# Performance work log

Measured on AMD Instinct MI355X. Metric: run time of the kernel, lower is better.

The kernel has to match this reference:

```python
import jax, jax.numpy as jnp
import numpy as np

NUM_HEADS = 16


def setup_inputs() -> dict:
    key = jax.random.key(0)
    k1, k2, k3, k4 = jax.random.split(key, 4)
    B, N, C = 2, 2048, 1024
    x = jax.random.normal(k1, (B, N, C), dtype=jnp.float32)
    mask = jax.random.randint(k2, (B, N), 0, 2) > 0  # bool [B, N]
    # torch Linear weights: y = x @ W.T
    w_qkv = jax.random.normal(k3, (3 * C, C), dtype=jnp.float32) * (C ** -0.5)
    w_proj = jax.random.normal(k4, (C, C), dtype=jnp.float32) * (C ** -0.5)
    b_proj = jnp.zeros((C,), dtype=jnp.float32)
    return {"x": x, "mask": mask, "w_qkv": w_qkv, "w_proj": w_proj, "b_proj": b_proj}


def reference(x, mask, w_qkv, w_proj, b_proj):
    B, N, C = x.shape
    H = NUM_HEADS
    D = C // H
    scale = D ** -0.5
    qkv = x @ w_qkv.T                                   # [B, N, 3C]
    qkv = qkv.reshape(B, N, 3, H, D).transpose(2, 0, 3, 1, 4)  # [3, B, H, N, D]
    q, k, v = qkv[0], qkv[1], qkv[2]
    attn = jnp.einsum('bhnd,bhmd->bhnm', q, k) * scale  # [B, H, N, N]
    mask_value = -jnp.finfo(attn.dtype).max
    m2 = mask[:, None, :] & mask[:, :, None]            # [B, N, N]
    attn = jnp.where(m2[:, None, :, :], attn, mask_value)
    attn = jax.nn.softmax(attn, axis=-1)
    # dropout layers are identity in eval mode
    out = jnp.einsum('bhnm,bhmd->bhnd', attn, v)        # [B, H, N, D]
    out = out.transpose(0, 2, 1, 3).reshape(B, N, C)
    out = out @ w_proj.T + b_proj
    return out
```

## Files before the change

kernel.cpp:

```cpp
#include <hip/hip_runtime.h>

typedef unsigned short u16;
typedef unsigned int   u32;
typedef short  short8 __attribute__((ext_vector_type(8)));
typedef float  f32x4  __attribute__((ext_vector_type(4)));
typedef float  f32x16 __attribute__((ext_vector_type(16)));
typedef u16    u16x4  __attribute__((ext_vector_type(4)));

__device__ __forceinline__ u16 f2b(float f) {
    u32 u = __float_as_uint(f);
    u32 r = (u + 0x7fffu + ((u >> 16) & 1u)) >> 16;
    return (u16)r;
}

__device__ __forceinline__ u32 cvtpk(float a, float b) {
    u32 r;
    asm("v_cvt_pk_bf16_f32 %0, %1, %2" : "=v"(r) : "v"(a), "v"(b));
    return r;
}

__device__ __forceinline__ void gload_lds16(const void* g, void* l) {
    __builtin_amdgcn_global_load_lds(
        (const __attribute__((address_space(1))) u32*)g,
        (__attribute__((address_space(3))) u32*)l,
        16, 0, 0);
}

__global__ void cvt_bf16(const float* __restrict__ src, u16* __restrict__ dst, int n4) {
    int i = blockIdx.x * blockDim.x + threadIdx.x;
    if (i >= n4) return;
    float4 v = ((const float4*)src)[i];
    u16x4 r = { f2b(v.x), f2b(v.y), f2b(v.z), f2b(v.w) };
    ((u16x4*)dst)[i] = r;
}

__global__ __launch_bounds__(256) void gemm_bt(
    const u16* __restrict__ A, const u16* __restrict__ Bm,
    u16* __restrict__ Cb, float* __restrict__ Cf, const float* __restrict__ bias,
    int M, int N, int K)
{
    __shared__ __align__(16) u16 As[128*32];
    __shared__ __align__(16) u16 Bs[128*32];
    const int t = threadIdx.x;
    const int w = t >> 6, lane = t & 63;
    const int l15 = lane & 15, lg = lane >> 4;
    const int m0 = blockIdx.y * 128, n0 = blockIdx.x * 128;
    const int wr = w >> 1, wc = w & 1;
    f32x4 acc[4][4] = {};

    for (int kt = 0; kt < K; kt += 32) {
        #pragma unroll
        for (int j = 0; j < 2; ++j) {
            const int c   = j*256 + t;
            const int row = c >> 2, colb = (c & 3) * 8;
            gload_lds16(&A [(size_t)(m0+row)*K + kt + colb], &As[(size_t)(j*256 + w*64)*8]);
            gload_lds16(&Bm[(size_t)(n0+row)*K + kt + colb], &Bs[(size_t)(j*256 + w*64)*8]);
        }
        __syncthreads();
        short8 af[4], bfr[4];
        #pragma unroll
        for (int mi = 0; mi < 4; ++mi)
            af[mi] = *(const short8*)&As[(wr*64 + mi*16 + l15)*32 + lg*8];
        #pragma unroll
        for (int ni = 0; ni < 4; ++ni)
            bfr[ni] = *(const short8*)&Bs[(wc*64 + ni*16 + l15)*32 + lg*8];
        #pragma unroll
        for (int mi = 0; mi < 4; ++mi)
            #pragma unroll
            for (int ni = 0; ni < 4; ++ni)
                acc[mi][ni] = __builtin_amdgcn_mfma_f32_16x16x32_bf16(af[mi], bfr[ni], acc[mi][ni], 0, 0, 0);
        __syncthreads();
    }

    #pragma unroll
    for (int mi = 0; mi < 4; ++mi) {
        #pragma unroll
        for (int ni = 0; ni < 4; ++ni) {
            const int row = m0 + wr*64 + mi*16 + lg*4;
            const int col = n0 + wc*64 + ni*16 + l15;
            if (Cb) {
                #pragma unroll
                for (int r = 0; r < 4; ++r)
                    Cb[(size_t)(row+r)*N + col] = f2b(acc[mi][ni][r]);
            } else {
                const float bv = bias ? bias[col] : 0.f;
                #pragma unroll
                for (int r = 0; r < 4; ++r)
                    Cf[(size_t)(row+r)*N + col] = acc[mi][ni][r] + bv;
            }
        }
    }
}

__global__ __launch_bounds__(256) void attn_v2(
    const u16* __restrict__ qkv,
    const int* __restrict__ mask,
    u16* __restrict__ aout)
{
    __shared__ __align__(16) u16 Ks[64*64];
    __shared__ __align__(16) u16 Vt[64*64];

    const int t = threadIdx.x, w = t >> 6, lane = t & 63;
    const int l31 = lane & 31, hi = lane >> 5;

    const int wid = ((blockIdx.x & 7) << 6) | (blockIdx.x >> 3);
    const int qt = wid & 15, h = (wid >> 4) & 15, b = wid >> 8;
    const int q0 = qt * 128 + w * 32;

    const size_t qrow = (size_t)(b*2048 + q0 + l31);
    short8 qf[4];
    #pragma unroll
    for (int i = 0; i < 4; ++i)
        qf[i] = *(const short8*)&qkv[qrow*3072 + h*64 + i*16 + hi*8];
    const int mq = mask[b*2048 + q0 + l31];

    float m_run = -3e38f, l_run = 0.f;
    f32x16 oacc[2] = {};

    const int vrr = t >> 3, vc8 = t & 7;
    short8 vreg0 = *(const short8*)&qkv[(size_t)(b*2048 +      vrr)*3072 + 2048 + h*64 + vc8*8];
    short8 vreg1 = *(const short8*)&qkv[(size_t)(b*2048 + 32 + vrr)*3072 + 2048 + h*64 + vc8*8];

    for (int kv0 = 0; kv0 < 2048; kv0 += 64) {
        __syncthreads();
        #pragma unroll
        for (int p = 0; p < 2; ++p) {
            const int kv = p*32 + vrr;
            const int kvhi = kv >> 3, kvlo = kv & 7;
            const short8 v = p ? vreg1 : vreg0;
            #pragma unroll
            for (int j = 0; j < 8; ++j)
                Vt[(vc8*8 + j)*64 + ((kvhi ^ ((j ^ vc8) & 7)) << 3) + kvlo] = (u16)v[j];
        }
        #pragma unroll
        for (int i = 0; i < 2; ++i) {
            const int row = w*16 + i*8 + (lane >> 3);
            const int sc  = (lane & 7) ^ (lane >> 3);
            gload_lds16(&qkv[(size_t)(b*2048 + kv0 + row)*3072 + 1024 + h*64 + sc*8],
                        &Ks[(w*16 + i*8)*64]);
        }
        const unsigned long long bal = __ballot(mask[b*2048 + kv0 + lane] != 0);
        const u32 mwA = (u32)bal, mwB = (u32)(bal >> 32);
        __syncthreads();

        if (kv0 + 64 < 2048) {
            vreg0 = *(const short8*)&qkv[(size_t)(b*2048 + kv0+64 + vrr)*3072 + 2048 + h*64 + vc8*8];
            vreg1 = *(const short8*)&qkv[(size_t)(b*2048 + kv0+96 + vrr)*3072 + 2048 + h*64 + vc8*8];
        }

        f32x16 st0 = {}, st1 = {};
        #pragma unroll
        for (int kd = 0; kd < 4; ++kd) {
            const int c = (2*kd + hi) ^ (l31 & 7);
            short8 kf0 = *(const short8*)&Ks[ l31      *64 + c*8];
            short8 kf1 = *(const short8*)&Ks[(32 + l31)*64 + c*8];
            st0 = __builtin_amdgcn_mfma_f32_32x32x16_bf16(kf0, qf[kd], st0, 0, 0, 0);
            st1 = __builtin_amdgcn_mfma_f32_32x32x16_bf16(kf1, qf[kd], st1, 0, 0, 0);
        }

        const u32 km0 = (mq ? mwA : 0u) >> (hi*4);
        const u32 km1 = (mq ? mwB : 0u) >> (hi*4);
        #pragma unroll
        for (int r = 0; r < 16; ++r) {
            const int pat = (r & 3) + 8*(r >> 2);
            const float t0 = ((km0 >> pat) & 1u) ? 0.f : -3e38f;
            const float t1 = ((km1 >> pat) & 1u) ? 0.f : -3e38f;
            st0[r] = fmaf(st0[r], 0.125f, t0);
            st1[r] = fmaf(st1[r], 0.125f, t1);
        }

        float pm0 = -3e38f, pm1 = -3e38f, pm2 = -3e38f, pm3 = -3e38f;
        #pragma unroll
        for (int r = 0; r < 16; r += 4) {
            pm0 = fmaxf(pm0, fmaxf(st0[r],   st1[r]));
            pm1 = fmaxf(pm1, fmaxf(st0[r+1], st1[r+1]));
            pm2 = fmaxf(pm2, fmaxf(st0[r+2], st1[r+2]));
            pm3 = fmaxf(pm3, fmaxf(st0[r+3], st1[r+3]));
        }
        float pm = fmaxf(fmaxf(pm0, pm1), fmaxf(pm2, pm3));
        pm = fmaxf(pm, __shfl_xor(pm, 32));
        const float m_new = fmaxf(m_run, pm);
        const float alpha = __expf(m_run - m_new);
        float rs0 = 0.f, rs1 = 0.f;
        #pragma unroll
        for (int r = 0; r < 16; ++r) {
            const float p0 = __expf(st0[r] - m_new);
            const float p1 = __expf(st1[r] - m_new);
            st0[r] = p0; st1[r] = p1;
            rs0 += p0; rs1 += p1;
        }
        float rs = rs0 + rs1;
        rs += __shfl_xor(rs, 32);
        l_run = l_run * alpha + rs;
        m_run = m_new;

        u32 o_[16], x_[16];
        #pragma unroll
        for (int m = 0; m < 8; ++m) {
            o_[m]     = cvtpk(st0[2*m], st0[2*m+1]);
            o_[8 + m] = cvtpk(st1[2*m], st1[2*m+1]);
        }
        #pragma unroll
        for (int m = 0; m < 16; ++m) x_[m] = (u32)__shfl_xor((int)o_[m], 32);

        #pragma unroll
        for (int r = 0; r < 16; ++r) {
            const int pat = (r & 3) + 8*(r >> 2);
            const float ar = __shfl(alpha, pat + 4*hi);
            oacc[0][r] *= ar; oacc[1][r] *= ar;
        }

        #pragma unroll
        for (int kk = 0; kk < 4; ++kk) {
            const int s8 = (kk >> 1) * 8, q4 = (kk & 1) * 4;
            union { u32 u[4]; short8 s; } pa;
            pa.u[0] = hi ? x_[s8+q4+2] : o_[s8+q4];
            pa.u[1] = hi ? x_[s8+q4+3] : o_[s8+q4+1];
            pa.u[2] = hi ? o_[s8+q4+2] : x_[s8+q4];
            pa.u[3] = hi ? o_[s8+q4+3] : x_[s8+q4+1];
            #pragma unroll
            for (int dt = 0; dt < 2; ++dt) {
                const int d = dt*32 + l31;
                const int c = (2*kk + hi) ^ ((d ^ (d >> 3)) & 7);
                short8 vf = *(const short8*)&Vt[d*64 + c*8];
                oacc[dt] = __builtin_amdgcn_mfma_f32_32x32x16_bf16(pa.s, vf, oacc[dt], 0, 0, 0);
            }
        }
    }

    const float inv = 1.f / l_run;
    #pragma unroll
    for (int r = 0; r < 16; ++r) {
        const int pat = (r & 3) + 8*(r >> 2);
        const float ir = __shfl(inv, pat + 4*hi);
        const size_t rowg = (size_t)(b*2048 + q0 + pat + 4*hi);
        aout[rowg*1024 + h*64 +      l31] = f2b(oacc[0][r] * ir);
        aout[rowg*1024 + h*64 + 32 + l31] = f2b(oacc[1][r] * ir);
    }
}

extern "C" void kernel_launch(void* const* d_in, const int* in_sizes, int n_in,
                              void* d_out, int out_size, void* d_ws, size_t ws_size,
                              hipStream_t stream)
{
    (void)in_sizes; (void)n_in; (void)out_size; (void)ws_size;
    const float* x      = (const float*)d_in[0];
    const int*   mask   = (const int*)  d_in[1];
    const float* w_qkv  = (const float*)d_in[2];
    const float* w_proj = (const float*)d_in[3];
    const float* b_proj = (const float*)d_in[4];
    float* out = (float*)d_out;

    const int M = 4096;
    const int C = 1024;

    u16* xb   = (u16*)d_ws;
    u16* wqb  = xb   + (size_t)M*C;
    u16* wpb  = wqb  + (size_t)3*C*C;
    u16* qkvb = wpb  + (size_t)C*C;
    u16* aob  = qkvb + (size_t)M*3*C;

    cvt_bf16<<<dim3((M*C/4   + 255)/256), 256, 0, stream>>>(x,      xb,  M*C/4);
    cvt_bf16<<<dim3((3*C*C/4 + 255)/256), 256, 0, stream>>>(w_qkv,  wqb, 3*C*C/4);
    cvt_bf16<<<dim3((C*C/4   + 255)/256), 256, 0, stream>>>(w_proj, wpb, C*C/4);

    gemm_bt<<<dim3(3*C/128, M/128), 256, 0, stream>>>(xb, wqb, qkvb, nullptr, nullptr, M, 3*C, C);
    attn_v2<<<dim3(512), 256, 0, stream>>>(qkvb, mask, aob);
    gemm_bt<<<dim3(C/128, M/128), 256, 0, stream>>>(aob, wpb, nullptr, out, b_proj, M, C, C);
}
```

Before: 172.1 us.

## Split attention KV range in two halves with a separate merge kernel

Splits the attention kernel's key/value loop into two halves, launched as 1024 blocks instead of 512, so more blocks are in flight to fill the GPU's compute units. Each half writes an unnormalized partial output in bf16 plus its running max and sum, reusing freed workspace buffers. A new elementwise merge kernel rescales and combines the two partials. The cost is an extra launch, extra global traffic for the partials, and some precision loss from storing unnormalized partials in bf16.

Measured after the change: 178.9 us. +4.0%, slower.

```diff
diff --git a/kernel.cpp b/kernel.cpp
--- a/kernel.cpp
+++ b/kernel.cpp
@@ -2,6 +2,7 @@
 
 typedef unsigned short u16;
 typedef unsigned int   u32;
+typedef unsigned long long u64;
 typedef short  short8 __attribute__((ext_vector_type(8)));
 typedef float  f32x4  __attribute__((ext_vector_type(4)));
 typedef float  f32x16 __attribute__((ext_vector_type(16)));
@@ -92,10 +93,11 @@
     }
 }
 
-__global__ __launch_bounds__(256) void attn_v2(
+__global__ __launch_bounds__(256) void attn_half(
     const u16* __restrict__ qkv,
     const int* __restrict__ mask,
-    u16* __restrict__ aout)
+    u16* __restrict__ pO0, u16* __restrict__ pO1,
+    float* __restrict__ pM, float* __restrict__ pL)
 {
     __shared__ __align__(16) u16 Ks[64*64];
     __shared__ __align__(16) u16 Vt[64*64];
@@ -103,9 +105,12 @@
     const int t = threadIdx.x, w = t >> 6, lane = t & 63;
     const int l31 = lane & 31, hi = lane >> 5;
 
-    const int wid = ((blockIdx.x & 7) << 6) | (blockIdx.x >> 3);
+    const int half  = blockIdx.x >> 9;
+    const int inner = blockIdx.x & 511;
+    const int wid = ((inner & 7) << 6) | (inner >> 3);
     const int qt = wid & 15, h = (wid >> 4) & 15, b = wid >> 8;
     const int q0 = qt * 128 + w * 32;
+    const int kvbase = half * 1024, kvend = kvbase + 1024;
 
     const size_t qrow = (size_t)(b*2048 + q0 + l31);
     short8 qf[4];
@@ -118,10 +123,10 @@
     f32x16 oacc[2] = {};
 
     const int vrr = t >> 3, vc8 = t & 7;
-    short8 vreg0 = *(const short8*)&qkv[(size_t)(b*2048 +      vrr)*3072 + 2048 + h*64 + vc8*8];
-    short8 vreg1 = *(const short8*)&qkv[(size_t)(b*2048 + 32 + vrr)*3072 + 2048 + h*64 + vc8*8];
-
-    for (int kv0 = 0; kv0 < 2048; kv0 += 64) {
+    short8 vreg0 = *(const short8*)&qkv[(size_t)(b*2048 + kvbase +      vrr)*3072 + 2048 + h*64 + vc8*8];
+    short8 vreg1 = *(const short8*)&qkv[(size_t)(b*2048 + kvbase + 32 + vrr)*3072 + 2048 + h*64 + vc8*8];
+
+    for (int kv0 = kvbase; kv0 < kvend; kv0 += 64) {
         __syncthreads();
         #pragma unroll
         for (int p = 0; p < 2; ++p) {
@@ -143,7 +148,7 @@
         const u32 mwA = (u32)bal, mwB = (u32)(bal >> 32);
         __syncthreads();
 
-        if (kv0 + 64 < 2048) {
+        if (kv0 + 64 < kvend) {
             vreg0 = *(const short8*)&qkv[(size_t)(b*2048 + kv0+64 + vrr)*3072 + 2048 + h*64 + vc8*8];
             vreg1 = *(const short8*)&qkv[(size_t)(b*2048 + kv0+96 + vrr)*3072 + 2048 + h*64 + vc8*8];
         }
@@ -228,15 +233,36 @@
         }
     }
 
-    const float inv = 1.f / l_run;
+    u16* __restrict__ pO = half ? pO1 : pO0;
+    if (hi == 0) {
+        const int rid = (b*2048 + q0 + l31)*16 + h;
+        pM[half*65536 + rid] = m_run;
+        pL[half*65536 + rid] = l_run;
+    }
     #pragma unroll
     for (int r = 0; r < 16; ++r) {
         const int pat = (r & 3) + 8*(r >> 2);
-        const float ir = __shfl(inv, pat + 4*hi);
-        const size_t rowg = (size_t)(b*2048 + q0 + pat + 4*hi);
-        aout[rowg*1024 + h*64 +      l31] = f2b(oacc[0][r] * ir);
-        aout[rowg*1024 + h*64 + 32 + l31] = f2b(oacc[1][r] * ir);
-    }
+        const int rid = (b*2048 + q0 + pat + 4*hi)*16 + h;
+        pO[(size_t)rid*64 +      l31] = f2b(oacc[0][r]);
+        pO[(size_t)rid*64 + 32 + l31] = f2b(oacc[1][r]);
+    }
+}
+
+__global__ __launch_bounds__(256) void attn_merge(
+    const u16* __restrict__ pO0, const u16* __restrict__ pO1,
+    const float* __restrict__ pM, const float* __restrict__ pL,
+    u16* __restrict__ aout)
+{
+    const int idx = blockIdx.x * 256 + threadIdx.x;
+    const int rid = idx >> 6;
+    const float m0 = pM[rid], m1 = pM[65536 + rid];
+    const float l0 = pL[rid], l1 = pL[65536 + rid];
+    const float mS = fmaxf(m0, m1);
+    const float a0 = __expf(m0 - mS), a1 = __expf(m1 - mS);
+    const float inv = 1.f / (l0*a0 + l1*a1);
+    const float o0 = __uint_as_float((u32)pO0[idx] << 16);
+    const float o1 = __uint_as_float((u32)pO1[idx] << 16);
+    aout[idx] = f2b((o0*a0 + o1*a1) * inv);
 }
 
 extern "C" void kernel_launch(void* const* d_in, const int* in_sizes, int n_in,
@@ -260,11 +286,17 @@
     u16* qkvb = wpb  + (size_t)C*C;
     u16* aob  = qkvb + (size_t)M*3*C;
 
+    u16*   pO0 = xb;
+    u16*   pO1 = aob;
+    float* pM  = (float*)wqb;
+    float* pL  = pM + 2*65536;
+
     cvt_bf16<<<dim3((M*C/4   + 255)/256), 256, 0, stream>>>(x,      xb,  M*C/4);
     cvt_bf16<<<dim3((3*C*C/4 + 255)/256), 256, 0, stream>>>(w_qkv,  wqb, 3*C*C/4);
     cvt_bf16<<<dim3((C*C/4   + 255)/256), 256, 0, stream>>>(w_proj, wpb, C*C/4);
 
     gemm_bt<<<dim3(3*C/128, M/128), 256, 0, stream>>>(xb, wqb, qkvb, nullptr, nullptr, M, 3*C, C);
-    attn_v2<<<dim3(512), 256, 0, stream>>>(qkvb, mask, aob);
+    attn_half<<<dim3(1024), 256, 0, stream>>>(qkvb, mask, pO0, pO1, pM, pL);
+    attn_merge<<<dim3(4096*1024/256), 256, 0, stream>>>(pO0, pO1, pM, pL, aob);
     gemm_bt<<<dim3(C/128, M/128), 256, 0, stream>>>(aob, wpb, nullptr, out, b_proj, M, C, C);
 }
```

## Double-buffer K/V tiles in attention kernel with one barrier per iteration

Applied to the files above, without the earlier changes.

The attention kernel now keeps two LDS buffers for K and transposed V. While the current tile is being computed, it writes the next tile into the other buffer and prefetches V registers and the mask two tiles ahead. The two __syncthreads per iteration become a single s_barrier with explicit waitcnt. It also moves the cross-half shuffles of the P fragments into the PV loop to lower register pressure. In exchange it doubles LDS use and relies on hand-tuned vmcnt counts, which are fragile.

After: 172.9 us. Within noise of the previous version (+0.5%).

```diff
diff --git a/kernel.cpp b/kernel.cpp
--- a/kernel.cpp
+++ b/kernel.cpp
@@ -2,6 +2,7 @@
 
 typedef unsigned short u16;
 typedef unsigned int   u32;
+typedef unsigned long long u64;
 typedef short  short8 __attribute__((ext_vector_type(8)));
 typedef float  f32x4  __attribute__((ext_vector_type(4)));
 typedef float  f32x16 __attribute__((ext_vector_type(16)));
@@ -92,13 +93,13 @@
     }
 }
 
-__global__ __launch_bounds__(256) void attn_v2(
+__global__ __launch_bounds__(256) void attn_v4(
     const u16* __restrict__ qkv,
     const int* __restrict__ mask,
     u16* __restrict__ aout)
 {
-    __shared__ __align__(16) u16 Ks[64*64];
-    __shared__ __align__(16) u16 Vt[64*64];
+    __shared__ __align__(16) u16 Ks[2][64*64];
+    __shared__ __align__(16) u16 Vt[2][64*64];
 
     const int t = threadIdx.x, w = t >> 6, lane = t & 63;
     const int l31 = lane & 31, hi = lane >> 5;
@@ -106,54 +107,89 @@
     const int wid = ((blockIdx.x & 7) << 6) | (blockIdx.x >> 3);
     const int qt = wid & 15, h = (wid >> 4) & 15, b = wid >> 8;
     const int q0 = qt * 128 + w * 32;
-
-    const size_t qrow = (size_t)(b*2048 + q0 + l31);
+    const int kvb = b * 2048;
+
+    const size_t qrow = (size_t)(kvb + q0 + l31);
     short8 qf[4];
     #pragma unroll
     for (int i = 0; i < 4; ++i)
         qf[i] = *(const short8*)&qkv[qrow*3072 + h*64 + i*16 + hi*8];
-    const int mq = mask[b*2048 + q0 + l31];
+    const int mq = mask[kvb + q0 + l31];
 
     float m_run = -3e38f, l_run = 0.f;
     f32x16 oacc[2] = {};
 
     const int vrr = t >> 3, vc8 = t & 7;
-    short8 vreg0 = *(const short8*)&qkv[(size_t)(b*2048 +      vrr)*3072 + 2048 + h*64 + vc8*8];
-    short8 vreg1 = *(const short8*)&qkv[(size_t)(b*2048 + 32 + vrr)*3072 + 2048 + h*64 + vc8*8];
-
-    for (int kv0 = 0; kv0 < 2048; kv0 += 64) {
-        __syncthreads();
-        #pragma unroll
-        for (int p = 0; p < 2; ++p) {
-            const int kv = p*32 + vrr;
+    const int sc  = (lane & 7) ^ (lane >> 3);
+    const int kri = lane >> 3;
+
+    short8 vnx0, vnx1;
+    {
+        const u16* p = qkv + (size_t)(kvb + vrr)*3072 + 2048 + h*64 + vc8*8;
+        vnx0 = *(const short8*)p;
+        vnx1 = *(const short8*)(p + (size_t)32*3072);
+    }
+    int mcur = mask[kvb + lane];
+    #pragma unroll
+    for (int pp = 0; pp < 2; ++pp) {
+        const int kv = pp*32 + vrr;
+        const int kvhi = kv >> 3, kvlo = kv & 7;
+        const short8 v = pp ? vnx1 : vnx0;
+        #pragma unroll
+        for (int j = 0; j < 8; ++j)
+            Vt[0][(vc8*8 + j)*64 + ((kvhi ^ ((j ^ vc8) & 7)) << 3) + kvlo] = (u16)v[j];
+    }
+    #pragma unroll
+    for (int i = 0; i < 2; ++i)
+        gload_lds16(&qkv[(size_t)(kvb + w*16 + i*8 + kri)*3072 + 1024 + h*64 + sc*8],
+                    &Ks[0][(w*16 + i*8)*64]);
+    __builtin_amdgcn_sched_barrier(0);
+    {
+        const u16* p = qkv + (size_t)(kvb + 64 + vrr)*3072 + 2048 + h*64 + vc8*8;
+        vnx0 = *(const short8*)p;
+        vnx1 = *(const short8*)(p + (size_t)32*3072);
+    }
+    asm volatile("s_waitcnt vmcnt(2) lgkmcnt(0)" ::: "memory");
+    __builtin_amdgcn_s_barrier();
+    __builtin_amdgcn_sched_barrier(0);
+
+    for (int it = 0; it < 32; ++it) {
+        u16* __restrict__ KsB = Ks[it & 1];
+        u16* __restrict__ VtB = Vt[it & 1];
+        u16* __restrict__ KsN = Ks[(it & 1) ^ 1];
+        u16* __restrict__ VtN = Vt[(it & 1) ^ 1];
+        const int tn1 = (it + 1 < 32 ? it + 1 : 31) * 64;
+        const int tn2 = (it + 2 < 32 ? it + 2 : 31) * 64;
+
+        #pragma unroll
+        for (int pp = 0; pp < 2; ++pp) {
+            const int kv = pp*32 + vrr;
             const int kvhi = kv >> 3, kvlo = kv & 7;
-            const short8 v = p ? vreg1 : vreg0;
+            const short8 v = pp ? vnx1 : vnx0;
             #pragma unroll
             for (int j = 0; j < 8; ++j)
-                Vt[(vc8*8 + j)*64 + ((kvhi ^ ((j ^ vc8) & 7)) << 3) + kvlo] = (u16)v[j];
-        }
-        #pragma unroll
-        for (int i = 0; i < 2; ++i) {
-            const int row = w*16 + i*8 + (lane >> 3);
-            const int sc  = (lane & 7) ^ (lane >> 3);
-            gload_lds16(&qkv[(size_t)(b*2048 + kv0 + row)*3072 + 1024 + h*64 + sc*8],
-                        &Ks[(w*16 + i*8)*64]);
-        }
-        const unsigned long long bal = __ballot(mask[b*2048 + kv0 + lane] != 0);
+                VtN[(vc8*8 + j)*64 + ((kvhi ^ ((j ^ vc8) & 7)) << 3) + kvlo] = (u16)v[j];
+        }
+        #pragma unroll
+        for (int i = 0; i < 2; ++i)
+            gload_lds16(&qkv[(size_t)(kvb + tn1 + w*16 + i*8 + kri)*3072 + 1024 + h*64 + sc*8],
+                        &KsN[(w*16 + i*8)*64]);
+        __builtin_amdgcn_sched_barrier(0);
+        {
+            const u16* p = qkv + (size_t)(kvb + tn2 + vrr)*3072 + 2048 + h*64 + vc8*8;
+            vnx0 = *(const short8*)p;
+            vnx1 = *(const short8*)(p + (size_t)32*3072);
+        }
+        const int mnew = mask[kvb + tn1 + lane];
+        const u64 bal = __ballot(mcur != 0);
         const u32 mwA = (u32)bal, mwB = (u32)(bal >> 32);
-        __syncthreads();
-
-        if (kv0 + 64 < 2048) {
-            vreg0 = *(const short8*)&qkv[(size_t)(b*2048 + kv0+64 + vrr)*3072 + 2048 + h*64 + vc8*8];
-            vreg1 = *(const short8*)&qkv[(size_t)(b*2048 + kv0+96 + vrr)*3072 + 2048 + h*64 + vc8*8];
-        }
 
         f32x16 st0 = {}, st1 = {};
         #pragma unroll
         for (int kd = 0; kd < 4; ++kd) {
             const int c = (2*kd + hi) ^ (l31 & 7);
-            short8 kf0 = *(const short8*)&Ks[ l31      *64 + c*8];
-            short8 kf1 = *(const short8*)&Ks[(32 + l31)*64 + c*8];
+            short8 kf0 = *(const short8*)&KsB[ l31      *64 + c*8];
+            short8 kf1 = *(const short8*)&KsB[(32 + l31)*64 + c*8];
             st0 = __builtin_amdgcn_mfma_f32_32x32x16_bf16(kf0, qf[kd], st0, 0, 0, 0);
             st1 = __builtin_amdgcn_mfma_f32_32x32x16_bf16(kf1, qf[kd], st1, 0, 0, 0);
         }
@@ -194,14 +230,12 @@
         l_run = l_run * alpha + rs;
         m_run = m_new;
 
-        u32 o_[16], x_[16];
+        u32 o_[16];
         #pragma unroll
         for (int m = 0; m < 8; ++m) {
             o_[m]     = cvtpk(st0[2*m], st0[2*m+1]);
             o_[8 + m] = cvtpk(st1[2*m], st1[2*m+1]);
         }
-        #pragma unroll
-        for (int m = 0; m < 16; ++m) x_[m] = (u32)__shfl_xor((int)o_[m], 32);
 
         #pragma unroll
         for (int r = 0; r < 16; ++r) {
@@ -212,20 +246,29 @@
 
         #pragma unroll
         for (int kk = 0; kk < 4; ++kk) {
-            const int s8 = (kk >> 1) * 8, q4 = (kk & 1) * 4;
+            const int base = (kk >> 1)*8 + (kk & 1)*4;
+            const u32 x0 = (u32)__shfl_xor((int)o_[base],   32);
+            const u32 x1 = (u32)__shfl_xor((int)o_[base+1], 32);
+            const u32 x2 = (u32)__shfl_xor((int)o_[base+2], 32);
+            const u32 x3 = (u32)__shfl_xor((int)o_[base+3], 32);
             union { u32 u[4]; short8 s; } pa;
-            pa.u[0] = hi ? x_[s8+q4+2] : o_[s8+q4];
-            pa.u[1] = hi ? x_[s8+q4+3] : o_[s8+q4+1];
-            pa.u[2] = hi ? o_[s8+q4+2] : x_[s8+q4];
-            pa.u[3] = hi ? o_[s8+q4+3] : x_[s8+q4+1];
+            pa.u[0] = hi ? x2 : o_[base];
+            pa.u[1] = hi ? x3 : o_[base+1];
+            pa.u[2] = hi ? o_[base+2] : x0;
+            pa.u[3] = hi ? o_[base+3] : x1;
             #pragma unroll
             for (int dt = 0; dt < 2; ++dt) {
                 const int d = dt*32 + l31;
                 const int c = (2*kk + hi) ^ ((d ^ (d >> 3)) & 7);
-                short8 vf = *(const short8*)&Vt[d*64 + c*8];
+                short8 vf = *(const short8*)&VtB[d*64 + c*8];
                 oacc[dt] = __builtin_amdgcn_mfma_f32_32x32x16_bf16(pa.s, vf, oacc[dt], 0, 0, 0);
             }
         }
+
+        mcur = mnew;
+        asm volatile("s_waitcnt vmcnt(3) lgkmcnt(0)" ::: "memory");
+        __builtin_amdgcn_s_barrier();
+        __builtin_amdgcn_sched_barrier(0);
     }
 
     const float inv = 1.f / l_run;
@@ -233,7 +276,7 @@
     for (int r = 0; r < 16; ++r) {
         const int pat = (r & 3) + 8*(r >> 2);
         const float ir = __shfl(inv, pat + 4*hi);
-        const size_t rowg = (size_t)(b*2048 + q0 + pat + 4*hi);
+        const size_t rowg = (size_t)(kvb + q0 + pat + 4*hi);
         aout[rowg*1024 + h*64 +      l31] = f2b(oacc[0][r] * ir);
         aout[rowg*1024 + h*64 + 32 + l31] = f2b(oacc[1][r] * ir);
     }
@@ -265,6 +308,6 @@
     cvt_bf16<<<dim3((C*C/4   + 255)/256), 256, 0, stream>>>(w_proj, wpb, C*C/4);
 
     gemm_bt<<<dim3(3*C/128, M/128), 256, 0, stream>>>(xb, wqb, qkvb, nullptr, nullptr, M, 3*C, C);
-    attn_v2<<<dim3(512), 256, 0, stream>>>(qkvb, mask, aob);
+    attn_v4<<<dim3(512), 256, 0, stream>>>(qkvb, mask, aob);
     gemm_bt<<<dim3(C/128, M/128), 256, 0, stream>>>(aob, wpb, nullptr, out, b_proj, M, C, C);
 }
```

## Fold mask into MFMA bias, use exp2 softmax with lazy rescaling

Applied to the files above, without the earlier changes.

Applies the key mask as an extra MFMA that adds a large negative bf16 bias to masked columns, replacing the per-element select-and-fma loop. Softmax switches to base-2 exponentials with the scale folded into one fma, and the running-max rescale of the output accumulator is skipped unless some row's max grows beyond a threshold. Query-row masking is handled by zeroing the scale factor. Cross-half shuffles are moved into the PV loop to cut register pressure. Deferred rescaling trades exactness for skipping work and relies on the threshold keeping exponentials in range.

New measurement: 158.3 us. 8.0% less time.

```diff
diff --git a/kernel.cpp b/kernel.cpp
--- a/kernel.cpp
+++ b/kernel.cpp
@@ -2,6 +2,7 @@
 
 typedef unsigned short u16;
 typedef unsigned int   u32;
+typedef unsigned long long u64;
 typedef short  short8 __attribute__((ext_vector_type(8)));
 typedef float  f32x4  __attribute__((ext_vector_type(4)));
 typedef float  f32x16 __attribute__((ext_vector_type(16)));
@@ -16,6 +17,12 @@
 __device__ __forceinline__ u32 cvtpk(float a, float b) {
     u32 r;
     asm("v_cvt_pk_bf16_f32 %0, %1, %2" : "=v"(r) : "v"(a), "v"(b));
+    return r;
+}
+
+__device__ __forceinline__ float ex2(float x) {
+    float r;
+    asm("v_exp_f32 %0, %1" : "=v"(r) : "v"(x));
     return r;
 }
 
@@ -92,7 +99,7 @@
     }
 }
 
-__global__ __launch_bounds__(256) void attn_v2(
+__global__ __launch_bounds__(256) void attn_v5(
     const u16* __restrict__ qkv,
     const int* __restrict__ mask,
     u16* __restrict__ aout)
@@ -113,8 +120,13 @@
     for (int i = 0; i < 4; ++i)
         qf[i] = *(const short8*)&qkv[qrow*3072 + h*64 + i*16 + hi*8];
     const int mq = mask[b*2048 + q0 + l31];
-
-    float m_run = -3e38f, l_run = 0.f;
+    const float qs2 = mq ? 0.18033688011f : 0.f;
+
+    union { u32 u[4]; short8 s; } qe;
+    qe.u[0] = hi ? 0u : 0x3F80u;
+    qe.u[1] = 0; qe.u[2] = 0; qe.u[3] = 0;
+
+    float m2 = -3e38f, l_run = 0.f;
     f32x16 oacc[2] = {};
 
     const int vrr = t >> 3, vc8 = t & 7;
@@ -139,7 +151,7 @@
             gload_lds16(&qkv[(size_t)(b*2048 + kv0 + row)*3072 + 1024 + h*64 + sc*8],
                         &Ks[(w*16 + i*8)*64]);
         }
-        const unsigned long long bal = __ballot(mask[b*2048 + kv0 + lane] != 0);
+        const u64 bal = __ballot(mask[b*2048 + kv0 + lane] != 0);
         const u32 mwA = (u32)bal, mwB = (u32)(bal >> 32);
         __syncthreads();
 
@@ -157,16 +169,14 @@
             st0 = __builtin_amdgcn_mfma_f32_32x32x16_bf16(kf0, qf[kd], st0, 0, 0, 0);
             st1 = __builtin_amdgcn_mfma_f32_32x32x16_bf16(kf1, qf[kd], st1, 0, 0, 0);
         }
-
-        const u32 km0 = (mq ? mwA : 0u) >> (hi*4);
-        const u32 km1 = (mq ? mwB : 0u) >> (hi*4);
-        #pragma unroll
-        for (int r = 0; r < 16; ++r) {
-            const int pat = (r & 3) + 8*(r >> 2);
-            const float t0 = ((km0 >> pat) & 1u) ? 0.f : -3e38f;
-            const float t1 = ((km1 >> pat) & 1u) ? 0.f : -3e38f;
-            st0[r] = fmaf(st0[r], 0.125f, t0);
-            st1[r] = fmaf(st1[r], 0.125f, t1);
+        {
+            union { u32 u[4]; short8 s; } ba0, ba1;
+            ba0.u[0] = (((mwA >> l31) & 1u) | (u32)hi) ? 0u : 0xFF7Fu;
+            ba1.u[0] = (((mwB >> l31) & 1u) | (u32)hi) ? 0u : 0xFF7Fu;
+            ba0.u[1] = 0; ba0.u[2] = 0; ba0.u[3] = 0;
+            ba1.u[1] = 0; ba1.u[2] = 0; ba1.u[3] = 0;
+            st0 = __builtin_amdgcn_mfma_f32_32x32x16_bf16(ba0.s, qe.s, st0, 0, 0, 0);
+            st1 = __builtin_amdgcn_mfma_f32_32x32x16_bf16(ba1.s, qe.s, st1, 0, 0, 0);
         }
 
         float pm0 = -3e38f, pm1 = -3e38f, pm2 = -3e38f, pm3 = -3e38f;
@@ -177,47 +187,54 @@
             pm2 = fmaxf(pm2, fmaxf(st0[r+2], st1[r+2]));
             pm3 = fmaxf(pm3, fmaxf(st0[r+3], st1[r+3]));
         }
-        float pm = fmaxf(fmaxf(pm0, pm1), fmaxf(pm2, pm3));
-        pm = fmaxf(pm, __shfl_xor(pm, 32));
-        const float m_new = fmaxf(m_run, pm);
-        const float alpha = __expf(m_run - m_new);
-        float rs0 = 0.f, rs1 = 0.f;
+        const float pmx = fmaxf(fmaxf(pm0, pm1), fmaxf(pm2, pm3));
+
+        if (__any(fmaf(pmx, qs2, -m2) > 11.5f)) {
+            float pml = pmx * qs2;
+            pml = fmaxf(pml, __shfl_xor(pml, 32));
+            const float m_new = fmaxf(m2, pml);
+            const float alpha = ex2(m2 - m_new);
+            l_run *= alpha;
+            #pragma unroll
+            for (int r = 0; r < 16; ++r) {
+                const int pat = (r & 3) + 8*(r >> 2);
+                const float ar = __shfl(alpha, pat + 4*hi);
+                oacc[0][r] *= ar; oacc[1][r] *= ar;
+            }
+            m2 = m_new;
+        }
+
+        const float nm = -m2;
+        float rs = 0.f;
         #pragma unroll
         for (int r = 0; r < 16; ++r) {
-            const float p0 = __expf(st0[r] - m_new);
-            const float p1 = __expf(st1[r] - m_new);
+            const float p0 = ex2(fmaf(st0[r], qs2, nm));
+            const float p1 = ex2(fmaf(st1[r], qs2, nm));
             st0[r] = p0; st1[r] = p1;
-            rs0 += p0; rs1 += p1;
-        }
-        float rs = rs0 + rs1;
+            rs += p0 + p1;
+        }
         rs += __shfl_xor(rs, 32);
-        l_run = l_run * alpha + rs;
-        m_run = m_new;
-
-        u32 o_[16], x_[16];
+        l_run += rs;
+
+        u32 o_[16];
         #pragma unroll
         for (int m = 0; m < 8; ++m) {
             o_[m]     = cvtpk(st0[2*m], st0[2*m+1]);
             o_[8 + m] = cvtpk(st1[2*m], st1[2*m+1]);
         }
-        #pragma unroll
-        for (int m = 0; m < 16; ++m) x_[m] = (u32)__shfl_xor((int)o_[m], 32);
-
-        #pragma unroll
-        for (int r = 0; r < 16; ++r) {
-            const int pat = (r & 3) + 8*(r >> 2);
-            const float ar = __shfl(alpha, pat + 4*hi);
-            oacc[0][r] *= ar; oacc[1][r] *= ar;
-        }
 
         #pragma unroll
         for (int kk = 0; kk < 4; ++kk) {
-            const int s8 = (kk >> 1) * 8, q4 = (kk & 1) * 4;
+            const int base = (kk >> 1)*8 + (kk & 1)*4;
+            const u32 x0 = (u32)__shfl_xor((int)o_[base],   32);
+            const u32 x1 = (u32)__shfl_xor((int)o_[base+1], 32);
+            const u32 x2 = (u32)__shfl_xor((int)o_[base+2], 32);
+            const u32 x3 = (u32)__shfl_xor((int)o_[base+3], 32);
             union { u32 u[4]; short8 s; } pa;
-            pa.u[0] = hi ? x_[s8+q4+2] : o_[s8+q4];
-            pa.u[1] = hi ? x_[s8+q4+3] : o_[s8+q4+1];
-            pa.u[2] = hi ? o_[s8+q4+2] : x_[s8+q4];
-            pa.u[3] = hi ? o_[s8+q4+3] : x_[s8+q4+1];
+            pa.u[0] = hi ? x2 : o_[base];
+            pa.u[1] = hi ? x3 : o_[base+1];
+            pa.u[2] = hi ? o_[base+2] : x0;
+            pa.u[3] = hi ? o_[base+3] : x1;
             #pragma unroll
             for (int dt = 0; dt < 2; ++dt) {
                 const int d = dt*32 + l31;
@@ -265,6 +282,6 @@
     cvt_bf16<<<dim3((C*C/4   + 255)/256), 256, 0, stream>>>(w_proj, wpb, C*C/4);
 
     gemm_bt<<<dim3(3*C/128, M/128), 256, 0, stream>>>(xb, wqb, qkvb, nullptr, nullptr, M, 3*C, C);
-    attn_v2<<<dim3(512), 256, 0, stream>>>(qkvb, mask, aob);
+    attn_v5<<<dim3(512), 256, 0, stream>>>(qkvb, mask, aob);
     gemm_bt<<<dim3(C/128, M/128), 256, 0, stream>>>(aob, wpb, nullptr, out, b_proj, M, C, C);
 }
```
